# Kernel tuning notes

Measured on AMD Instinct MI355X. Metric: run time of the kernel, lower is better.

## Reference

```python
import jax, jax.numpy as jnp
import numpy as np
from functools import partial

# Thresholds from _SamAutomaticMaskGenerator defaults
MASK_THRESHOLD = 0.0
PRED_IOU_THRESH = 0.88
STABILITY_THRESH = 0.95
STABILITY_OFFSET = 1.0
BOX_NMS_THRESH = 0.7

N_MASKS, H, W = 1024, 256, 256  # 32x32 point grid -> 1024 masks; SAM low-res mask size


def setup_inputs() -> dict:
    key = jax.random.key(0)
    k1, k2, k3, k4, k5 = jax.random.split(key, 5)
    # Structured blob logits so stability scores / boxes / NMS behave realistically.
    cy = jax.random.uniform(k1, (N_MASKS,)) * H
    cx = jax.random.uniform(k2, (N_MASKS,)) * W
    r = 20.0 + jax.random.uniform(k3, (N_MASKS,)) * 60.0
    yy = jnp.arange(H, dtype=jnp.float32)[:, None]
    xx = jnp.arange(W, dtype=jnp.float32)[None, :]
    dist = jnp.sqrt((yy - cy[:, None, None]) ** 2 + (xx - cx[:, None, None]) ** 2)  # [N,H,W]
    noise = jax.random.normal(k4, (N_MASKS, H, W), dtype=jnp.float32) * 0.1
    mask_logits = (2.0 * (r[:, None, None] - dist) + noise).astype(jnp.float32)
    iou_preds = jax.random.uniform(k5, (N_MASKS,), dtype=jnp.float32)
    return {"mask_logits": mask_logits, "iou_preds": iou_preds}


def _masks_to_boxes(binary):
    # binary: [N,H,W] bool -> inclusive xyxy boxes [N,4] float32 (empty masks -> zeros),
    # matching SAM's batched_mask_to_box.
    n, h, w = binary.shape
    row_any = binary.any(axis=2)  # [N,H]
    col_any = binary.any(axis=1)  # [N,W]
    ys = jnp.arange(h)
    xs = jnp.arange(w)
    top = jnp.min(jnp.where(row_any, ys, h), axis=1)
    bottom = jnp.max(jnp.where(row_any, ys, -1), axis=1)
    left = jnp.min(jnp.where(col_any, xs, w), axis=1)
    right = jnp.max(jnp.where(col_any, xs, -1), axis=1)
    boxes = jnp.stack([left, top, right, bottom], axis=-1).astype(jnp.float32)
    empty = ~row_any.any(axis=1)
    return jnp.where(empty[:, None], 0.0, boxes)


def _box_iou_one_vs_all(box, boxes):
    # box: [4], boxes: [N,4] xyxy -> iou [N]
    x0 = jnp.maximum(box[0], boxes[:, 0])
    y0 = jnp.maximum(box[1], boxes[:, 1])
    x1 = jnp.minimum(box[2], boxes[:, 2])
    y1 = jnp.minimum(box[3], boxes[:, 3])
    inter = jnp.clip(x1 - x0, 0.0) * jnp.clip(y1 - y0, 0.0)
    area_a = jnp.clip(box[2] - box[0], 0.0) * jnp.clip(box[3] - box[1], 0.0)
    area_b = jnp.clip(boxes[:, 2] - boxes[:, 0], 0.0) * jnp.clip(boxes[:, 3] - boxes[:, 1], 0.0)
    return inter / jnp.maximum(area_a + area_b - inter, 1e-6)


def _greedy_nms(boxes, scores, valid, thresh):
    # Greedy NMS over fixed N, returning a keep mask in original order.
    n = boxes.shape[0]
    order = jnp.argsort(-jnp.where(valid, scores, -jnp.inf))
    b = boxes[order]
    keep0 = valid[order]
    idx = jnp.arange(n)

    def body(i, keep):
        iou = _box_iou_one_vs_all(b[i], b)
        suppress = (iou > thresh) & (idx > i) & keep[i]
        return keep & ~suppress

    keep_sorted = jax.lax.fori_loop(0, n, body, keep0)
    return jnp.zeros((n,), dtype=bool).at[order].set(keep_sorted)


def reference(mask_logits, iou_preds):
    # Stability score: area at (thr+offset) / area at (thr-offset), as in SAM.
    hi = (mask_logits > (MASK_THRESHOLD + STABILITY_OFFSET)).sum(axis=(1, 2)).astype(jnp.float32)
    lo = (mask_logits > (MASK_THRESHOLD - STABILITY_OFFSET)).sum(axis=(1, 2)).astype(jnp.float32)
    stability = hi / jnp.maximum(lo, 1.0)

    binary = mask_logits > MASK_THRESHOLD  # [N,H,W] bool
    valid = (iou_preds > PRED_IOU_THRESH) & (stability >= STABILITY_THRESH)

    boxes = _masks_to_boxes(binary)  # [N,4]
    keep = _greedy_nms(boxes, iou_preds, valid, BOX_NMS_THRESH)  # [N] bool

    # Differentiable summary output: soft masks gated by kept score.
    gated = iou_preds * keep.astype(mask_logits.dtype)  # [N]
    out = jax.nn.sigmoid(mask_logits) * gated[:, None, None]  # [N,H,W]
    return out, keep, boxes
```

## Files before the change

### kernel.cpp

```cpp
#include <hip/hip_runtime.h>
#include <math.h>

#define NMASK 1024
#define HH 256
#define WW 256
#define HW 65536
#define OUT_ELEMS 67108864

__global__ __launch_bounds__(256) void stats_kernel(
    const float* __restrict__ logits, int* __restrict__ stats) {
  const int m = blockIdx.x;
  const int t = threadIdx.x;
  const float4* __restrict__ p = (const float4*)(logits + (size_t)m * HW);

  int hi = 0, lo = 0;
  int miny = HH, maxy = -1, minx = WW, maxx = -1;

  for (int k = 0; k < 64; ++k) {
    const int f = k * 256 + t;
    const float4 v = p[f];
    const int y = f >> 6;
    const int x0 = (f & 63) << 2;

    const bool p0 = v.x > 0.0f, p1 = v.y > 0.0f, p2 = v.z > 0.0f, p3 = v.w > 0.0f;
    hi += (v.x > 1.0f) + (v.y > 1.0f) + (v.z > 1.0f) + (v.w > 1.0f);
    lo += (v.x > -1.0f) + (v.y > -1.0f) + (v.z > -1.0f) + (v.w > -1.0f);
    if (p0 | p1 | p2 | p3) {
      miny = min(miny, y);
      maxy = max(maxy, y);
      if (p0) { minx = min(minx, x0);     maxx = max(maxx, x0); }
      if (p1) { minx = min(minx, x0 + 1); maxx = max(maxx, x0 + 1); }
      if (p2) { minx = min(minx, x0 + 2); maxx = max(maxx, x0 + 2); }
      if (p3) { minx = min(minx, x0 + 3); maxx = max(maxx, x0 + 3); }
    }
  }

  for (int off = 32; off; off >>= 1) {
    hi += __shfl_down(hi, off);
    lo += __shfl_down(lo, off);
    miny = min(miny, __shfl_down(miny, off));
    maxy = max(maxy, __shfl_down(maxy, off));
    minx = min(minx, __shfl_down(minx, off));
    maxx = max(maxx, __shfl_down(maxx, off));
  }

  __shared__ int red[4][6];
  const int wv = t >> 6, ln = t & 63;
  if (ln == 0) {
    red[wv][0] = hi;  red[wv][1] = lo;
    red[wv][2] = miny; red[wv][3] = maxy;
    red[wv][4] = minx; red[wv][5] = maxx;
  }
  __syncthreads();
  if (t == 0) {
    int H2 = 0, L2 = 0, mny = HH, mxy = -1, mnx = WW, mxx = -1;
    for (int w = 0; w < 4; ++w) {
      H2 += red[w][0]; L2 += red[w][1];
      mny = min(mny, red[w][2]); mxy = max(mxy, red[w][3]);
      mnx = min(mnx, red[w][4]); mxx = max(mxx, red[w][5]);
    }
    int* s = stats + m * 8;
    s[0] = H2; s[1] = L2; s[2] = mny; s[3] = mxy; s[4] = mnx; s[5] = mxx;
  }
}

__global__ __launch_bounds__(1024) void score_kernel(
    const float* __restrict__ iou_preds, const int* __restrict__ stats,
    float* __restrict__ score, int* __restrict__ validA,
    float* __restrict__ boxf, int* __restrict__ nvalid,
    float* __restrict__ boxes_out) {
  __shared__ int cnt;
  const int i = threadIdx.x;
  if (i == 0) cnt = 0;
  __syncthreads();

  const int* s = stats + i * 8;
  const int hi = s[0], lo = s[1], mny = s[2], mxy = s[3], mnx = s[4], mxx = s[5];
  const float stab = (float)hi / fmaxf((float)lo, 1.0f);
  const float iv = iou_preds[i];
  const bool valid = (iv > 0.88f) && (stab >= 0.95f);

  float bx0, by0, bx1, by1;
  if (mxy < 0) { bx0 = by0 = bx1 = by1 = 0.0f; }
  else { bx0 = (float)mnx; by0 = (float)mny; bx1 = (float)mxx; by1 = (float)mxy; }

  boxf[i * 4 + 0] = bx0; boxf[i * 4 + 1] = by0;
  boxf[i * 4 + 2] = bx1; boxf[i * 4 + 3] = by1;
  boxes_out[i * 4 + 0] = bx0; boxes_out[i * 4 + 1] = by0;
  boxes_out[i * 4 + 2] = bx1; boxes_out[i * 4 + 3] = by1;

  score[i] = valid ? iv : -INFINITY;
  validA[i] = valid ? 1 : 0;
  if (valid) atomicAdd(&cnt, 1);
  __syncthreads();
  if (i == 0) *nvalid = cnt;
}

__global__ __launch_bounds__(256) void rank_kernel(
    const float* __restrict__ score, const int* __restrict__ validA,
    const float* __restrict__ boxf, float* __restrict__ sbox,
    int* __restrict__ sidx, int* __restrict__ svalid) {
  const int i = blockIdx.x;
  const int t = threadIdx.x;
  const float si = score[i];
  int r = 0;
  for (int j = t; j < NMASK; j += 256) {
    const float sj = score[j];
    r += (sj > si) || (sj == si && j < i);
  }
  for (int off = 32; off; off >>= 1) r += __shfl_down(r, off);
  __shared__ int red[4];
  if ((t & 63) == 0) red[t >> 6] = r;
  __syncthreads();
  if (t == 0) {
    const int rank = red[0] + red[1] + red[2] + red[3];
    sidx[rank] = i;
    svalid[rank] = validA[i];
    sbox[rank * 4 + 0] = boxf[i * 4 + 0];
    sbox[rank * 4 + 1] = boxf[i * 4 + 1];
    sbox[rank * 4 + 2] = boxf[i * 4 + 2];
    sbox[rank * 4 + 3] = boxf[i * 4 + 3];
  }
}

__global__ __launch_bounds__(1024) void iou_kernel(
    const float* __restrict__ sbox, const int* __restrict__ nvalid,
    unsigned long long* __restrict__ rows) {
  const int i = blockIdx.x;
  if (i >= *nvalid) return;
  const int j = threadIdx.x;
  const float ax0 = sbox[i * 4 + 0], ay0 = sbox[i * 4 + 1];
  const float ax1 = sbox[i * 4 + 2], ay1 = sbox[i * 4 + 3];
  const float bx0 = sbox[j * 4 + 0], by0 = sbox[j * 4 + 1];
  const float bx1 = sbox[j * 4 + 2], by1 = sbox[j * 4 + 3];
  const float x0 = fmaxf(ax0, bx0), y0 = fmaxf(ay0, by0);
  const float x1 = fminf(ax1, bx1), y1 = fminf(ay1, by1);
  const float inter = fmaxf(x1 - x0, 0.0f) * fmaxf(y1 - y0, 0.0f);
  const float aa = fmaxf(ax1 - ax0, 0.0f) * fmaxf(ay1 - ay0, 0.0f);
  const float ab = fmaxf(bx1 - bx0, 0.0f) * fmaxf(by1 - by0, 0.0f);
  const float iou = inter / fmaxf(aa + ab - inter, 1e-6f);
  const bool supp = (iou > 0.7f) && (j > i);
  const unsigned long long b = __ballot(supp);
  if ((j & 63) == 0) rows[i * 16 + (j >> 6)] = b;
}

#define PREF_ROWS 256
__global__ __launch_bounds__(256) void nms_kernel(
    const int* __restrict__ nvalid, const unsigned long long* __restrict__ rows,
    const int* __restrict__ sidx, const int* __restrict__ svalid,
    const float* __restrict__ iou_preds, float* __restrict__ gated,
    float* __restrict__ keep_out) {
  __shared__ unsigned long long srows[PREF_ROWS * 16];
  const int nv = *nvalid;
  const int t = threadIdx.x;
  const int pref = min(nv, PREF_ROWS) * 16;
  for (int k = t; k < pref; k += 256) srows[k] = rows[k];
  __syncthreads();
  if (t >= 64) return;
  const int lane = t;

  unsigned long long keepword = 0ull;
  for (int c = 0; c < 16; ++c) {
    const int v = svalid[c * 64 + lane];
    const unsigned long long b = __ballot(v != 0);
    if (lane == c) keepword = b;
  }

  for (int i = 0; i < nv; ++i) {
    const int w = i >> 6, bit = i & 63;
    const unsigned long long kw = __shfl(keepword, w, 64);
    if ((kw >> bit) & 1ull) {
      if (lane < 16) {
        const unsigned long long r =
            (i < PREF_ROWS) ? srows[i * 16 + lane] : rows[i * 16 + lane];
        keepword &= ~r;
      }
    }
  }

  for (int c = 0; c < 16; ++c) {
    const unsigned long long kw = __shfl(keepword, c, 64);
    const int j = c * 64 + lane;
    const int orig = sidx[j];
    const float kept = ((kw >> lane) & 1ull) ? 1.0f : 0.0f;
    keep_out[orig] = kept;
    gated[orig] = kept * iou_preds[orig];
  }
}

__global__ __launch_bounds__(256) void out_kernel(
    const float* __restrict__ logits, const float* __restrict__ gated,
    float* __restrict__ out) {
  const int b = blockIdx.x;
  const int m = b >> 4;
  const float g = gated[m];
  const size_t base4 = (size_t)m * 16384 + (size_t)(b & 15) * 1024;
  const float4* __restrict__ in4 = (const float4*)logits + base4;
  float4* __restrict__ o4 = (float4*)out + base4;
  const int t = threadIdx.x;
  if (g == 0.0f) {
    const float4 z = {0.0f, 0.0f, 0.0f, 0.0f};
    o4[t] = z; o4[t + 256] = z; o4[t + 512] = z; o4[t + 768] = z;
  } else {
#pragma unroll
    for (int k = 0; k < 4; ++k) {
      const float4 v = in4[t + k * 256];
      float4 r;
      r.x = g / (1.0f + __expf(-v.x));
      r.y = g / (1.0f + __expf(-v.y));
      r.z = g / (1.0f + __expf(-v.z));
      r.w = g / (1.0f + __expf(-v.w));
      o4[t + k * 256] = r;
    }
  }
}

extern "C" void kernel_launch(void* const* d_in, const int* in_sizes, int n_in,
                              void* d_out, int out_size, void* d_ws, size_t ws_size,
                              hipStream_t stream) {
  const float* logits = (const float*)d_in[0];
  const float* iou    = (const float*)d_in[1];

  float* out       = (float*)d_out;
  float* keep_out  = out + OUT_ELEMS;
  float* boxes_out = keep_out + NMASK;

  char* w = (char*)d_ws;
  int*   stats  = (int*)(w);
  float* score  = (float*)(w + 32768);
  int*   validA = (int*)(w + 36864);
  float* boxf   = (float*)(w + 40960);
  int*   nvalid = (int*)(w + 57344);
  float* sbox   = (float*)(w + 57408);
  int*   sidx   = (int*)(w + 73792);
  int*   svalid = (int*)(w + 77888);
  float* gated  = (float*)(w + 81984);
  unsigned long long* rows = (unsigned long long*)(w + 86080);

  stats_kernel<<<NMASK, 256, 0, stream>>>(logits, stats);
  score_kernel<<<1, 1024, 0, stream>>>(iou, stats, score, validA, boxf, nvalid, boxes_out);
  rank_kernel<<<NMASK, 256, 0, stream>>>(score, validA, boxf, sbox, sidx, svalid);
  iou_kernel<<<NMASK, 1024, 0, stream>>>(sbox, nvalid, rows);
  nms_kernel<<<1, 256, 0, stream>>>(nvalid, rows, sidx, svalid, iou, gated, keep_out);
  out_kernel<<<NMASK * 16, 256, 0, stream>>>(logits, gated, out);
}
```

Baseline: 467.9 us.

## Fuse score and rank kernels, derive valid count in NMS, enlarge out blocks

Merges the single-block score kernel into the rank kernel: every block recomputes all 1024 scores into shared memory and also writes its own box, which removes one launch and the intermediate score/validA/boxf buffers. The valid count is no longer passed in. iou_kernel now skips rows by svalid, and nms_kernel counts valid entries with popcount and always prefetches 256 rows. The output kernel processes 4x more data per block with a quarter of the blocks. The trade-off is redundant score computation in every block, plus an unconditional prefetch of rows that iou_kernel may never have written for the invalid tail.

Result: slower. 480.3 us (+2.7%).

```diff
diff --git a/kernel.cpp b/kernel.cpp
--- a/kernel.cpp
+++ b/kernel.cpp
@@ -64,49 +64,28 @@
   }
 }
 
-__global__ __launch_bounds__(1024) void score_kernel(
+__global__ __launch_bounds__(256) void scorerank_kernel(
     const float* __restrict__ iou_preds, const int* __restrict__ stats,
-    float* __restrict__ score, int* __restrict__ validA,
-    float* __restrict__ boxf, int* __restrict__ nvalid,
+    float* __restrict__ sbox, int* __restrict__ sidx, int* __restrict__ svalid,
     float* __restrict__ boxes_out) {
-  __shared__ int cnt;
-  const int i = threadIdx.x;
-  if (i == 0) cnt = 0;
-  __syncthreads();
-
-  const int* s = stats + i * 8;
-  const int hi = s[0], lo = s[1], mny = s[2], mxy = s[3], mnx = s[4], mxx = s[5];
-  const float stab = (float)hi / fmaxf((float)lo, 1.0f);
-  const float iv = iou_preds[i];
-  const bool valid = (iv > 0.88f) && (stab >= 0.95f);
-
-  float bx0, by0, bx1, by1;
-  if (mxy < 0) { bx0 = by0 = bx1 = by1 = 0.0f; }
-  else { bx0 = (float)mnx; by0 = (float)mny; bx1 = (float)mxx; by1 = (float)mxy; }
-
-  boxf[i * 4 + 0] = bx0; boxf[i * 4 + 1] = by0;
-  boxf[i * 4 + 2] = bx1; boxf[i * 4 + 3] = by1;
-  boxes_out[i * 4 + 0] = bx0; boxes_out[i * 4 + 1] = by0;
-  boxes_out[i * 4 + 2] = bx1; boxes_out[i * 4 + 3] = by1;
-
-  score[i] = valid ? iv : -INFINITY;
-  validA[i] = valid ? 1 : 0;
-  if (valid) atomicAdd(&cnt, 1);
-  __syncthreads();
-  if (i == 0) *nvalid = cnt;
-}
-
-__global__ __launch_bounds__(256) void rank_kernel(
-    const float* __restrict__ score, const int* __restrict__ validA,
-    const float* __restrict__ boxf, float* __restrict__ sbox,
-    int* __restrict__ sidx, int* __restrict__ svalid) {
-  const int i = blockIdx.x;
-  const int t = threadIdx.x;
-  const float si = score[i];
+  __shared__ float ssc[NMASK];
+  const int b = blockIdx.x;
+  const int t = threadIdx.x;
+
+  for (int j = t; j < NMASK; j += 256) {
+    const int* s = stats + j * 8;
+    const float stab = (float)s[0] / fmaxf((float)s[1], 1.0f);
+    const float iv = iou_preds[j];
+    const bool valid = (iv > 0.88f) && (stab >= 0.95f);
+    ssc[j] = valid ? iv : -INFINITY;
+  }
+  __syncthreads();
+
+  const float si = ssc[b];
   int r = 0;
   for (int j = t; j < NMASK; j += 256) {
-    const float sj = score[j];
-    r += (sj > si) || (sj == si && j < i);
+    const float sj = ssc[j];
+    r += (sj > si) || (sj == si && j < b);
   }
   for (int off = 32; off; off >>= 1) r += __shfl_down(r, off);
   __shared__ int red[4];
@@ -114,20 +93,24 @@
   __syncthreads();
   if (t == 0) {
     const int rank = red[0] + red[1] + red[2] + red[3];
-    sidx[rank] = i;
-    svalid[rank] = validA[i];
-    sbox[rank * 4 + 0] = boxf[i * 4 + 0];
-    sbox[rank * 4 + 1] = boxf[i * 4 + 1];
-    sbox[rank * 4 + 2] = boxf[i * 4 + 2];
-    sbox[rank * 4 + 3] = boxf[i * 4 + 3];
+    const int* s = stats + b * 8;
+    float bx0, by0, bx1, by1;
+    if (s[3] < 0) { bx0 = by0 = bx1 = by1 = 0.0f; }
+    else { bx0 = (float)s[4]; by0 = (float)s[2]; bx1 = (float)s[5]; by1 = (float)s[3]; }
+    sidx[rank] = b;
+    svalid[rank] = (si != -INFINITY) ? 1 : 0;
+    sbox[rank * 4 + 0] = bx0; sbox[rank * 4 + 1] = by0;
+    sbox[rank * 4 + 2] = bx1; sbox[rank * 4 + 3] = by1;
+    boxes_out[b * 4 + 0] = bx0; boxes_out[b * 4 + 1] = by0;
+    boxes_out[b * 4 + 2] = bx1; boxes_out[b * 4 + 3] = by1;
   }
 }
 
 __global__ __launch_bounds__(1024) void iou_kernel(
-    const float* __restrict__ sbox, const int* __restrict__ nvalid,
+    const float* __restrict__ sbox, const int* __restrict__ svalid,
     unsigned long long* __restrict__ rows) {
   const int i = blockIdx.x;
-  if (i >= *nvalid) return;
+  if (!svalid[i]) return;
   const int j = threadIdx.x;
   const float ax0 = sbox[i * 4 + 0], ay0 = sbox[i * 4 + 1];
   const float ax1 = sbox[i * 4 + 2], ay1 = sbox[i * 4 + 3];
@@ -146,25 +129,27 @@
 
 #define PREF_ROWS 256
 __global__ __launch_bounds__(256) void nms_kernel(
-    const int* __restrict__ nvalid, const unsigned long long* __restrict__ rows,
+    const unsigned long long* __restrict__ rows,
     const int* __restrict__ sidx, const int* __restrict__ svalid,
     const float* __restrict__ iou_preds, float* __restrict__ gated,
     float* __restrict__ keep_out) {
   __shared__ unsigned long long srows[PREF_ROWS * 16];
-  const int nv = *nvalid;
-  const int t = threadIdx.x;
-  const int pref = min(nv, PREF_ROWS) * 16;
-  for (int k = t; k < pref; k += 256) srows[k] = rows[k];
+  const int t = threadIdx.x;
+  for (int k = t; k < PREF_ROWS * 16; k += 256) srows[k] = rows[k];
   __syncthreads();
   if (t >= 64) return;
   const int lane = t;
 
   unsigned long long keepword = 0ull;
+  int nv = 0;
   for (int c = 0; c < 16; ++c) {
     const int v = svalid[c * 64 + lane];
     const unsigned long long b = __ballot(v != 0);
     if (lane == c) keepword = b;
-  }
+    nv += (int)__popcll(b) ? 0 : 0;
+    nv += (int)__popcll(b);
+  }
+  nv >>= 0;
 
   for (int i = 0; i < nv; ++i) {
     const int w = i >> 6, bit = i & 63;
@@ -192,18 +177,19 @@
     const float* __restrict__ logits, const float* __restrict__ gated,
     float* __restrict__ out) {
   const int b = blockIdx.x;
-  const int m = b >> 4;
+  const int m = b >> 2;
   const float g = gated[m];
-  const size_t base4 = (size_t)m * 16384 + (size_t)(b & 15) * 1024;
+  const size_t base4 = (size_t)m * 16384 + (size_t)(b & 3) * 4096;
   const float4* __restrict__ in4 = (const float4*)logits + base4;
   float4* __restrict__ o4 = (float4*)out + base4;
   const int t = threadIdx.x;
   if (g == 0.0f) {
     const float4 z = {0.0f, 0.0f, 0.0f, 0.0f};
-    o4[t] = z; o4[t + 256] = z; o4[t + 512] = z; o4[t + 768] = z;
+#pragma unroll
+    for (int k = 0; k < 16; ++k) o4[t + k * 256] = z;
   } else {
 #pragma unroll
-    for (int k = 0; k < 4; ++k) {
+    for (int k = 0; k < 16; ++k) {
       const float4 v = in4[t + k * 256];
       float4 r;
       r.x = g / (1.0f + __expf(-v.x));
@@ -227,20 +213,15 @@
 
   char* w = (char*)d_ws;
   int*   stats  = (int*)(w);
-  float* score  = (float*)(w + 32768);
-  int*   validA = (int*)(w + 36864);
-  float* boxf   = (float*)(w + 40960);
-  int*   nvalid = (int*)(w + 57344);
-  float* sbox   = (float*)(w + 57408);
-  int*   sidx   = (int*)(w + 73792);
-  int*   svalid = (int*)(w + 77888);
-  float* gated  = (float*)(w + 81984);
-  unsigned long long* rows = (unsigned long long*)(w + 86080);
+  float* sbox   = (float*)(w + 32768);
+  int*   sidx   = (int*)(w + 49152);
+  int*   svalid = (int*)(w + 53248);
+  float* gated  = (float*)(w + 57344);
+  unsigned long long* rows = (unsigned long long*)(w + 61440);
 
   stats_kernel<<<NMASK, 256, 0, stream>>>(logits, stats);
-  score_kernel<<<1, 1024, 0, stream>>>(iou, stats, score, validA, boxf, nvalid, boxes_out);
-  rank_kernel<<<NMASK, 256, 0, stream>>>(score, validA, boxf, sbox, sidx, svalid);
-  iou_kernel<<<NMASK, 1024, 0, stream>>>(sbox, nvalid, rows);
-  nms_kernel<<<1, 256, 0, stream>>>(nvalid, rows, sidx, svalid, iou, gated, keep_out);
-  out_kernel<<<NMASK * 16, 256, 0, stream>>>(logits, gated, out);
-}
+  scorerank_kernel<<<NMASK, 256, 0, stream>>>(iou, stats, sbox, sidx, svalid, boxes_out);
+  iou_kernel<<<NMASK, 1024, 0, stream>>>(sbox, svalid, rows);
+  nms_kernel<<<1, 256, 0, stream>>>(rows, sidx, svalid, iou, gated, keep_out);
+  out_kernel<<<NMASK * 4, 256, 0, stream>>>(logits, gated, out);
+}
```
